# Optimization experiments

Measured on AMD Instinct MI355X. Metric: run time of the kernel, lower is better.

## Reference

```python
import jax, jax.numpy as jnp
import numpy as np

B, S, H, K, V = 1024, 50, 128, 4, 100000
ROUTING_TIMES = 3

def _squash(c):
    # c: [B,K,1,H]
    cap_norm = jnp.sum(jnp.square(c), -1, keepdims=True)
    scalar_factor = cap_norm / (1.0 + cap_norm) / jnp.sqrt(cap_norm + 1e-9)
    return scalar_factor * c

def setup_inputs() -> dict:
    key = jax.random.key(0)
    k1, k2, k3, k4, k5, k6 = jax.random.split(key, 6)
    item_seq = jax.random.randint(k1, (B, S), 0, V)
    mask = jax.random.randint(k2, (B, S), 0, 2).astype(jnp.float32)
    item = jax.random.randint(k3, (B, 1), 0, V)
    emb = jax.random.normal(k4, (V, H), dtype=jnp.float32) * 0.02
    W = jax.random.normal(k5, (H, H), dtype=jnp.float32) * (1.0 / np.sqrt(H))
    # bilinear_type==0 -> capsule routing logits initialized with randn
    capsule_weight0 = jax.random.normal(k6, (B, K, S), dtype=jnp.float32)
    return {"item_seq": item_seq, "mask": mask, "item": item,
            "emb": emb, "W": W, "capsule_weight0": capsule_weight0}

def reference(item_seq, mask, item, emb, W, capsule_weight0):
    # padding_idx=0: lookups see a zeroed row 0 (and get no grad there),
    # but calculate_loss uses the raw weight matrix.
    emb_lookup = emb.at[0].set(0.0)
    seq_emb = emb_lookup[item_seq]          # [B,S,H]
    item_e = emb_lookup[item[:, 0]]         # [B,H]  (squeeze(1))

    # CapsuleNetwork, bilinear_type==0: Linear(H,H,no bias) then repeat_interleave along hidden
    h = seq_emb @ W.T                        # [B,S,H]
    hat = jnp.repeat(h, K, axis=2)           # [B,S,H*K] (repeat_interleave semantics)
    hat = hat.reshape(B, S, K, H).transpose(0, 2, 1, 3)  # [B,K,S,H]
    hat_iter = jax.lax.stop_gradient(hat)    # stop_grad=True (detach)

    atten_mask = jnp.broadcast_to(mask[:, None, :], (B, K, S))
    cw = capsule_weight0
    cap = None
    for i in range(ROUTING_TIMES):
        # torch F.softmax with no dim on a 3-D tensor uses dim=0 (batch axis) -- faithful
        sw = jax.nn.softmax(cw, axis=0)
        sw = jnp.where(atten_mask == 0, 0.0, sw)[:, :, None, :]  # [B,K,1,S]
        src = hat_iter if i < ROUTING_TIMES - 1 else hat
        cap = _squash(sw @ src)                                   # [B,K,1,H]
        if i < ROUTING_TIMES - 1:
            delta = (hat_iter @ jnp.swapaxes(cap, 3, 2)).reshape(B, K, S)
            cw = cw + delta

    user_emb = cap.reshape(B, K, H)          # multi_interest_emb

    # hard readout: pick interest with max dot against target item
    cos = jnp.einsum('bkh,bh->bk', user_emb, item_e)
    k_index = jnp.argmax(cos, axis=1)        # [B]
    best = jnp.take_along_axis(user_emb, k_index[:, None, None], axis=1)[:, 0]  # [B,H]

    # cross-entropy over all items (raw embedding weight)
    scores = best @ emb.T                    # [B,V]
    logp = jax.nn.log_softmax(scores, axis=-1)
    loss = -jnp.mean(jnp.take_along_axis(logp, item, axis=1))
    return user_emb, loss
```

## Files before the change

kernel.cpp:

```cpp
#include <hip/hip_runtime.h>
#include <math.h>

#define BB 1024
#define SS 50
#define SSP 51
#define HH 128
#define KK 4
#define VV 100000
#define NVT 782
#define NVT8 784
#define VPAD (NVT8*128)
#define KS (KK*SS)
#define NHM 400
#define NCONV ((VPAD*HH)/1024)
#define NPAD_LAST 96.0f

typedef __attribute__((ext_vector_type(8))) short bf16x8;
typedef __attribute__((ext_vector_type(4))) float f32x4;

__device__ __forceinline__ ushort f2bf(float x) {
  unsigned u = __float_as_uint(x);
  unsigned r = u + 0x7FFF + ((u >> 16) & 1);
  return (ushort)(r >> 16);
}
__device__ __forceinline__ float bf2f(ushort u) {
  return __uint_as_float(((unsigned)u) << 16);
}
__device__ __forceinline__ bf16x8 cvt8(float4 a, float4 b) {
  bf16x8 r;
  r[0] = (short)f2bf(a.x); r[1] = (short)f2bf(a.y);
  r[2] = (short)f2bf(a.z); r[3] = (short)f2bf(a.w);
  r[4] = (short)f2bf(b.x); r[5] = (short)f2bf(b.y);
  r[6] = (short)f2bf(b.z); r[7] = (short)f2bf(b.w);
  return r;
}

__global__ __launch_bounds__(256) void k_pre(const float* __restrict__ emb,
                                             ushort* __restrict__ embb,
                                             const float* __restrict__ cw0,
                                             float* __restrict__ cm,
                                             float* __restrict__ s1,
                                             float* __restrict__ s2,
                                             float* __restrict__ accum,
                                             const int* __restrict__ item_seq,
                                             const float* __restrict__ W,
                                             ushort* __restrict__ hb16) {
  const int t = threadIdx.x;
  if (blockIdx.x < NHM) {
    __shared__ __align__(16) ushort sWf[32 * 512];
    const int w = t >> 6;
    const int lane = t & 63;
    const int lr = lane & 15;
    const int lq = lane >> 4;
    const int m0 = blockIdx.x * 128;

#pragma unroll
    for (int it = 0; it < 8; ++it) {
      int pos = t + it * 256;
      int ch = pos >> 6, l = pos & 63;
      int n = (ch & 7) * 16 + (l & 15);
      int k0 = (ch >> 3) * 32 + (l >> 4) * 8;
      float4 a = *(const float4*)&W[n * HH + k0];
      float4 b = *(const float4*)&W[n * HH + k0 + 4];
      *(bf16x8*)&sWf[ch * 512 + l * 8] = cvt8(a, b);
    }

    bf16x8 af[4][2];
#pragma unroll
    for (int vv = 0; vv < 2; ++vv) {
      int m = m0 + w * 32 + vv * 16 + lr;
      int idx = item_seq[m];
#pragma unroll
      for (int ks = 0; ks < 4; ++ks) {
        if (idx != 0) {
          float4 a = *(const float4*)&emb[(size_t)idx * HH + ks * 32 + lq * 8];
          float4 b = *(const float4*)&emb[(size_t)idx * HH + ks * 32 + lq * 8 + 4];
          af[ks][vv] = cvt8(a, b);
        } else {
          af[ks][vv] = (bf16x8){0, 0, 0, 0, 0, 0, 0, 0};
        }
      }
    }
    __syncthreads();

    f32x4 acc[8][2];
#pragma unroll
    for (int nt = 0; nt < 8; ++nt)
#pragma unroll
      for (int vv = 0; vv < 2; ++vv) acc[nt][vv] = (f32x4){0.f, 0.f, 0.f, 0.f};

#pragma unroll
    for (int ks = 0; ks < 4; ++ks) {
      bf16x8 bw[8];
#pragma unroll
      for (int nt = 0; nt < 8; ++nt)
        bw[nt] = *(const bf16x8*)&sWf[(ks * 8 + nt) * 512 + lane * 8];
#pragma unroll
      for (int nt = 0; nt < 8; ++nt)
#pragma unroll
        for (int vv = 0; vv < 2; ++vv)
          acc[nt][vv] = __builtin_amdgcn_mfma_f32_16x16x32_bf16(af[ks][vv], bw[nt], acc[nt][vv], 0, 0, 0);
    }

#pragma unroll
    for (int nt = 0; nt < 8; ++nt)
#pragma unroll
      for (int vv = 0; vv < 2; ++vv)
#pragma unroll
        for (int r = 0; r < 4; ++r) {
          int m = m0 + w * 32 + vv * 16 + lq * 4 + r;
          hb16[(size_t)m * HH + nt * 16 + lr] = f2bf(acc[nt][vv][r]);
        }
  } else if (blockIdx.x < NHM + KS) {
    __shared__ float red[256];
    const int c = blockIdx.x - NHM;
    if (t < 8) s1[t * KS + c] = 0.f;
    if (t >= 8 && t < 16) s2[(t - 8) * KS + c] = 0.f;
    if (c < 4) accum[c * 256 + t] = 0.f;
    float s = 0.f;
    for (int b = t; b < BB; b += 256) s += __expf(cw0[(size_t)b * KS + c]);
    red[t] = s;
    __syncthreads();
    for (int o = 128; o > 0; o >>= 1) {
      if (t < o) red[t] += red[t + o];
      __syncthreads();
    }
    if (t == 0) cm[c] = red[0];
  } else {
    size_t i = ((size_t)(blockIdx.x - NHM - KS) * 256 + t) * 4;
    ushort4 o;
    if (i < (size_t)VV * HH) {
      float4 v = *(const float4*)&emb[i];
      o = make_ushort4(f2bf(v.x), f2bf(v.y), f2bf(v.z), f2bf(v.w));
    } else {
      o = make_ushort4(0, 0, 0, 0);
    }
    *(ushort4*)&embb[i] = o;
  }
}

__global__ __launch_bounds__(256) void k_route(const float* __restrict__ cwsrc,
                                               float* __restrict__ cwdst,
                                               const ushort* __restrict__ hb16,
                                               const float* __restrict__ csum,
                                               int nslots,
                                               const float* __restrict__ mask,
                                               int last,
                                               float* __restrict__ out_ue,
                                               const float* __restrict__ emb,
                                               const int* __restrict__ item,
                                               ushort* __restrict__ bestb,
                                               float* __restrict__ csnext,
                                               float* __restrict__ si) {
  __shared__ ushort shT[128 * SSP];
  __shared__ float swl[KS];
  __shared__ float c32p[256];
  __shared__ float c32[128];
  __shared__ float csq[128];
  __shared__ float ie4r[32];
  __shared__ float ie4z[32];
  __shared__ float fac[4];
  __shared__ float cosk[4];
  __shared__ float cosr[4];
  __shared__ int kb;
  const int t = threadIdx.x;
  const int b = blockIdx.x;

  for (int p = t; p < (SS * HH) / 4; p += 256) {
    int flat = 4 * p;
    int s = flat >> 7, col = flat & 127;
    ushort4 v = *(const ushort4*)&hb16[(size_t)b * SS * HH + flat];
    shT[(col + 0) * SSP + s] = v.x;
    shT[(col + 1) * SSP + s] = v.y;
    shT[(col + 2) * SSP + s] = v.z;
    shT[(col + 3) * SSP + s] = v.w;
  }
  if (t < KS) {
    float den = 0.f;
    for (int g2 = 0; g2 < nslots; ++g2) den += csum[g2 * KS + t];
    float v = __expf(cwsrc[(size_t)b * KS + t]) / den;
    if (mask[b * SS + (t % SS)] == 0.0f) v = 0.0f;
    swl[t] = v;
  }
  __syncthreads();

  {
    int col = t & 127;
    int half = t >> 7;
    int k = col >> 5;
    float acc = 0.f;
    const float* swk = &swl[k * SS + half * 25];
    const ushort* hc = &shT[col * SSP + half * 25];
    for (int s = 0; s < 25; ++s) acc += swk[s] * bf2f(hc[s]);
    c32p[t] = acc;
  }
  __syncthreads();
  if (t < 128) c32[t] = c32p[t] + c32p[t + 128];
  __syncthreads();
  if (t < 4) {
    float nrm = 0.f;
#pragma unroll
    for (int j = 0; j < 32; ++j) { float c = c32[32 * t + j]; nrm += c * c; }
    nrm *= 4.0f;
    fac[t] = nrm / (1.0f + nrm) / sqrtf(nrm + 1e-9f);
  }
  __syncthreads();
  if (t < 128) csq[t] = c32[t] * fac[t >> 5];
  __syncthreads();

  if (!last) {
    if (t < KS) {
      int k = t / SS, s = t % SS;
      const float* cq = &csq[32 * k];
      float d = 0.f;
#pragma unroll
      for (int j = 0; j < 32; ++j) d += bf2f(shT[(32 * k + j) * SSP + s]) * cq[j];
      float nv = cwsrc[(size_t)b * KS + t] + 4.0f * d;
      cwdst[(size_t)b * KS + t] = nv;
      atomicAdd(&csnext[(b & 7) * KS + t], __expf(nv));
    }
  } else {
    for (int hh = t; hh < 512; hh += 256) {
      int k = hh >> 7, r = (hh & 127) >> 2;
      out_ue[(size_t)b * 512 + hh] = csq[32 * k + r];
    }
    if (t < 32) {
      int idx = item[b];
      const float* e = emb + (size_t)idx * HH + 4 * t;
      float v = e[0] + e[1] + e[2] + e[3];
      ie4r[t] = v;
      ie4z[t] = (idx == 0) ? 0.f : v;
    }
    __syncthreads();
    if (t < 4) {
      float cz = 0.f, cr = 0.f;
#pragma unroll
      for (int j = 0; j < 32; ++j) {
        cz += csq[32 * t + j] * ie4z[j];
        cr += csq[32 * t + j] * ie4r[j];
      }
      cosk[t] = cz; cosr[t] = cr;
    }
    __syncthreads();
    if (t == 0) {
      int kbest = 0; float bv = cosk[0];
#pragma unroll
      for (int k = 1; k < 4; ++k) if (cosk[k] > bv) { bv = cosk[k]; kbest = k; }
      kb = kbest;
      si[b] = cosr[kbest];
    }
    __syncthreads();
    if (t < 128) bestb[(size_t)b * HH + t] = f2bf(csq[32 * kb + (t >> 2)]);
  }
}

__global__ __launch_bounds__(256) void k_score_mfma(const ushort* __restrict__ bestb,
                                                    const ushort* __restrict__ embb,
                                                    float* __restrict__ accum) {
  const int lin = blockIdx.x;
  const int xcd = lin & 7;
  const int g = lin >> 3;
  const int sub = g & 15;
  const int bt8 = sub >> 1;
  const int vh = sub & 1;
  const int vt = xcd * (NVT8 / 8) + (g >> 4);
  if (vt >= NVT) return;

  __shared__ __align__(16) ushort sB[32 * 512];
  __shared__ float ssm[128][4];
  const int t = threadIdx.x;
  const int w = t >> 6;
  const int lane = t & 63;
  const int lr = lane & 15;
  const int lq = lane >> 4;
  const int b0 = bt8 * 128;
  const int v0 = vt * 128 + vh * 64 + w * 16;

  bf16x8 af[4];
#pragma unroll
  for (int ks = 0; ks < 4; ++ks)
    af[ks] = *(const bf16x8*)&embb[(size_t)(v0 + lr) * HH + ks * 32 + lq * 8];

#pragma unroll
  for (int it = 0; it < 8; ++it) {
    int pos = t + it * 256;
    int ch = pos >> 6;
    int l = pos & 63;
    int ks = ch >> 3, bt = ch & 7;
    *(bf16x8*)&sB[ch * 512 + l * 8] =
        *(const bf16x8*)&bestb[(size_t)(b0 + bt * 16 + (l & 15)) * HH + ks * 32 + (l >> 4) * 8];
  }
  __syncthreads();

#pragma unroll
  for (int bt = 0; bt < 8; ++bt) {
    bf16x8 bfr[4];
#pragma unroll
    for (int ks = 0; ks < 4; ++ks)
      bfr[ks] = *(const bf16x8*)&sB[(ks * 8 + bt) * 512 + lane * 8];
    f32x4 a = (f32x4){0.f, 0.f, 0.f, 0.f};
#pragma unroll
    for (int ks = 0; ks < 4; ++ks)
      a = __builtin_amdgcn_mfma_f32_16x16x32_bf16(af[ks], bfr[ks], a, 0, 0, 0);
    float s = __expf(a[0]) + __expf(a[1]) + __expf(a[2]) + __expf(a[3]);
    s += __shfl_xor(s, 16);
    s += __shfl_xor(s, 32);
    if (lq == 0) ssm[bt * 16 + lr][w] = s;
  }
  __syncthreads();
  if (t < 128) {
    float s = ssm[t][0] + ssm[t][1] + ssm[t][2] + ssm[t][3];
    atomicAdd(&accum[b0 + t], s);
  }
}

__global__ __launch_bounds__(256) void k_loss(const float* __restrict__ accum,
                                              const float* __restrict__ si,
                                              float* __restrict__ outloss) {
  __shared__ float red[256];
  const int t = threadIdx.x;
  float s = 0.f;
  for (int b = t; b < BB; b += 256)
    s += logf(accum[b] - NPAD_LAST) - si[b];
  red[t] = s;
  __syncthreads();
  for (int o = 128; o > 0; o >>= 1) {
    if (t < o) red[t] += red[t + o];
    __syncthreads();
  }
  if (t == 0) outloss[0] = red[0] / (float)BB;
}

extern "C" void kernel_launch(void* const* d_in, const int* in_sizes, int n_in,
                              void* d_out, int out_size, void* d_ws, size_t ws_size,
                              hipStream_t stream) {
  const int*   item_seq = (const int*)d_in[0];
  const float* mask     = (const float*)d_in[1];
  const int*   item     = (const int*)d_in[2];
  const float* emb      = (const float*)d_in[3];
  const float* W        = (const float*)d_in[4];
  const float* cw0      = (const float*)d_in[5];
  float* out = (float*)d_out;
  float* outloss = out + (size_t)BB * KK * HH;

  float* ws = (float*)d_ws;
  float* cm    = ws;
  float* s1    = cm + 256;
  float* s2    = s1 + 8 * KS;
  float* si    = s2 + 8 * KS;
  float* accum = si + BB;
  float* cw    = accum + BB;
  ushort* hb16  = (ushort*)(cw + (size_t)BB * KS);
  ushort* embb  = hb16 + (size_t)BB * SS * HH;
  ushort* bestb = embb + (size_t)VPAD * HH;

  k_pre<<<dim3(NHM + KS + NCONV), 256, 0, stream>>>(emb, embb, cw0, cm, s1, s2,
                                                    accum, item_seq, W, hb16);

  k_route<<<dim3(BB), 256, 0, stream>>>(cw0, cw, hb16, cm, 1, mask, 0, out, emb, item, bestb, s1, si);
  k_route<<<dim3(BB), 256, 0, stream>>>(cw, cw, hb16, s1, 8, mask, 0, out, emb, item, bestb, s2, si);
  k_route<<<dim3(BB), 256, 0, stream>>>(cw, cw, hb16, s2, 8, mask, 1, out, emb, item, bestb, s1, si);

  k_score_mfma<<<dim3(NVT8 * 16), 256, 0, stream>>>(bestb, embb, accum);
  k_loss<<<dim3(1), 256, 0, stream>>>(accum, si, outloss);
}
```

Measured before the change: 217.0 us.

## Fuse fp32-to-bf16 embedding conversion into score kernel and widen vocab tiles

Removes the separate pass that converts the full embedding table to a padded bf16 copy. The score kernel now loads fp32 embedding rows directly and converts them in registers. Each block covers 128 vocab rows (32 per wave, two MFMA row tiles) instead of 64, which halves the block count. It also prefetches the next k-slice of the B fragments from LDS. This avoids writing and re-reading a ~25MB bf16 table, at the cost of reading fp32 rows (twice the bytes) in the score kernel and using more registers.

```diff
diff --git a/kernel.cpp b/kernel.cpp
--- a/kernel.cpp
+++ b/kernel.cpp
@@ -9,10 +9,8 @@
 #define VV 100000
 #define NVT 782
 #define NVT8 784
-#define VPAD (NVT8*128)
 #define KS (KK*SS)
 #define NHM 400
-#define NCONV ((VPAD*HH)/1024)
 #define NPAD_LAST 96.0f
 
 typedef __attribute__((ext_vector_type(8))) short bf16x8;
@@ -36,7 +34,6 @@
 }
 
 __global__ __launch_bounds__(256) void k_pre(const float* __restrict__ emb,
-                                             ushort* __restrict__ embb,
                                              const float* __restrict__ cw0,
                                              float* __restrict__ cm,
                                              float* __restrict__ s1,
@@ -111,7 +108,7 @@
           int m = m0 + w * 32 + vv * 16 + lq * 4 + r;
           hb16[(size_t)m * HH + nt * 16 + lr] = f2bf(acc[nt][vv][r]);
         }
-  } else if (blockIdx.x < NHM + KS) {
+  } else {
     __shared__ float red[256];
     const int c = blockIdx.x - NHM;
     if (t < 8) s1[t * KS + c] = 0.f;
@@ -126,16 +123,6 @@
       __syncthreads();
     }
     if (t == 0) cm[c] = red[0];
-  } else {
-    size_t i = ((size_t)(blockIdx.x - NHM - KS) * 256 + t) * 4;
-    ushort4 o;
-    if (i < (size_t)VV * HH) {
-      float4 v = *(const float4*)&emb[i];
-      o = make_ushort4(f2bf(v.x), f2bf(v.y), f2bf(v.z), f2bf(v.w));
-    } else {
-      o = make_ushort4(0, 0, 0, 0);
-    }
-    *(ushort4*)&embb[i] = o;
   }
 }
 
@@ -255,15 +242,13 @@
 }
 
 __global__ __launch_bounds__(256) void k_score_mfma(const ushort* __restrict__ bestb,
-                                                    const ushort* __restrict__ embb,
+                                                    const float* __restrict__ emb,
                                                     float* __restrict__ accum) {
   const int lin = blockIdx.x;
   const int xcd = lin & 7;
   const int g = lin >> 3;
-  const int sub = g & 15;
-  const int bt8 = sub >> 1;
-  const int vh = sub & 1;
-  const int vt = xcd * (NVT8 / 8) + (g >> 4);
+  const int bt8 = g & 7;
+  const int vt = xcd * (NVT8 / 8) + (g >> 3);
   if (vt >= NVT) return;
 
   __shared__ __align__(16) ushort sB[32 * 512];
@@ -274,12 +259,25 @@
   const int lr = lane & 15;
   const int lq = lane >> 4;
   const int b0 = bt8 * 128;
-  const int v0 = vt * 128 + vh * 64 + w * 16;
-
-  bf16x8 af[4];
-#pragma unroll
-  for (int ks = 0; ks < 4; ++ks)
-    af[ks] = *(const bf16x8*)&embb[(size_t)(v0 + lr) * HH + ks * 32 + lq * 8];
+  const int v0 = vt * 128 + w * 32;
+
+  bf16x8 af[4][2];
+#pragma unroll
+  for (int vv = 0; vv < 2; ++vv) {
+    int row = v0 + vv * 16 + lr;
+    bool ok = row < VV;
+    const float* er = emb + (size_t)row * HH;
+#pragma unroll
+    for (int ks = 0; ks < 4; ++ks) {
+      if (ok) {
+        float4 a = *(const float4*)&er[ks * 32 + lq * 8];
+        float4 b = *(const float4*)&er[ks * 32 + lq * 8 + 4];
+        af[ks][vv] = cvt8(a, b);
+      } else {
+        af[ks][vv] = (bf16x8){0, 0, 0, 0, 0, 0, 0, 0};
+      }
+    }
+  }
 
 #pragma unroll
   for (int it = 0; it < 8; ++it) {
@@ -290,19 +288,46 @@
     *(bf16x8*)&sB[ch * 512 + l * 8] =
         *(const bf16x8*)&bestb[(size_t)(b0 + bt * 16 + (l & 15)) * HH + ks * 32 + (l >> 4) * 8];
   }
-  __syncthreads();
+
+  f32x4 acc[8][2];
+#pragma unroll
+  for (int bt = 0; bt < 8; ++bt)
+#pragma unroll
+    for (int vv = 0; vv < 2; ++vv) acc[bt][vv] = (f32x4){0.f, 0.f, 0.f, 0.f};
+
+  __syncthreads();
+
+  bf16x8 bcur[8];
+#pragma unroll
+  for (int bt = 0; bt < 8; ++bt)
+    bcur[bt] = *(const bf16x8*)&sB[bt * 512 + lane * 8];
+
+#pragma unroll
+  for (int ks = 0; ks < 4; ++ks) {
+    bf16x8 bnxt[8];
+    if (ks < 3) {
+#pragma unroll
+      for (int bt = 0; bt < 8; ++bt)
+        bnxt[bt] = *(const bf16x8*)&sB[((ks + 1) * 8 + bt) * 512 + lane * 8];
+    }
+#pragma unroll
+    for (int bt = 0; bt < 8; ++bt)
+#pragma unroll
+      for (int vv = 0; vv < 2; ++vv)
+        acc[bt][vv] = __builtin_amdgcn_mfma_f32_16x16x32_bf16(af[ks][vv], bcur[bt], acc[bt][vv], 0, 0, 0);
+    if (ks < 3) {
+#pragma unroll
+      for (int bt = 0; bt < 8; ++bt) bcur[bt] = bnxt[bt];
+    }
+  }
 
 #pragma unroll
   for (int bt = 0; bt < 8; ++bt) {
-    bf16x8 bfr[4];
-#pragma unroll
-    for (int ks = 0; ks < 4; ++ks)
-      bfr[ks] = *(const bf16x8*)&sB[(ks * 8 + bt) * 512 + lane * 8];
-    f32x4 a = (f32x4){0.f, 0.f, 0.f, 0.f};
-#pragma unroll
-    for (int ks = 0; ks < 4; ++ks)
-      a = __builtin_amdgcn_mfma_f32_16x16x32_bf16(af[ks], bfr[ks], a, 0, 0, 0);
-    float s = __expf(a[0]) + __expf(a[1]) + __expf(a[2]) + __expf(a[3]);
+    float s = 0.f;
+#pragma unroll
+    for (int vv = 0; vv < 2; ++vv)
+#pragma unroll
+      for (int r = 0; r < 4; ++r) s += __expf(acc[bt][vv][r]);
     s += __shfl_xor(s, 16);
     s += __shfl_xor(s, 32);
     if (lq == 0) ssm[bt * 16 + lr][w] = s;
@@ -351,16 +376,15 @@
   float* accum = si + BB;
   float* cw    = accum + BB;
   ushort* hb16  = (ushort*)(cw + (size_t)BB * KS);
-  ushort* embb  = hb16 + (size_t)BB * SS * HH;
-  ushort* bestb = embb + (size_t)VPAD * HH;
-
-  k_pre<<<dim3(NHM + KS + NCONV), 256, 0, stream>>>(emb, embb, cw0, cm, s1, s2,
-                                                    accum, item_seq, W, hb16);
+  ushort* bestb = hb16 + (size_t)BB * SS * HH;
+
+  k_pre<<<dim3(NHM + KS), 256, 0, stream>>>(emb, cw0, cm, s1, s2, accum,
+                                            item_seq, W, hb16);
 
   k_route<<<dim3(BB), 256, 0, stream>>>(cw0, cw, hb16, cm, 1, mask, 0, out, emb, item, bestb, s1, si);
   k_route<<<dim3(BB), 256, 0, stream>>>(cw, cw, hb16, s1, 8, mask, 0, out, emb, item, bestb, s2, si);
   k_route<<<dim3(BB), 256, 0, stream>>>(cw, cw, hb16, s2, 8, mask, 1, out, emb, item, bestb, s1, si);
 
-  k_score_mfma<<<dim3(NVT8 * 16), 256, 0, stream>>>(bestb, embb, accum);
+  k_score_mfma<<<dim3(NVT8 * 8), 256, 0, stream>>>(bestb, emb, accum);
   k_loss<<<dim3(1), 256, 0, stream>>>(accum, si, outloss);
 }
```

Result: no change. 215.9 us (-0.5%).
